# Optimization experiments

Measured on AMD Instinct MI355X. Metric: run time of the kernel, lower is better.

The kernel has to match this reference:

```python
import jax, jax.numpy as jnp
import numpy as np

B, H, W, C = 4, 64, 64, 128
C8 = C // 8  # query/key channels


def setup_inputs() -> dict:
    key = jax.random.key(0)
    ks = jax.random.split(key, 7)
    s_in = 1.0 / np.sqrt(C)
    x = jax.random.normal(ks[0], (B, H, W, C), dtype=jnp.float32)
    Wq = jax.random.normal(ks[1], (C, C8), dtype=jnp.float32) * s_in
    bq = jnp.zeros((C8,), dtype=jnp.float32)
    Wk = jax.random.normal(ks[2], (C, C8), dtype=jnp.float32) * s_in
    bk = jnp.zeros((C8,), dtype=jnp.float32)
    Wv = jax.random.normal(ks[3], (C, C), dtype=jnp.float32) * s_in
    bv = jnp.zeros((C,), dtype=jnp.float32)
    gamma = jnp.zeros((), dtype=jnp.float32)
    return {"x": x, "Wq": Wq, "bq": bq, "Wk": Wk, "bk": bk,
            "Wv": Wv, "bv": bv, "gamma": gamma}


def reference(x, Wq, bq, Wk, bk, Wv, bv, gamma):
    b, h, w, c = x.shape
    n = h * w
    xt = x.reshape(b, n, c)  # tokens
    # 1x1 convs == per-token linear projections
    q = xt @ Wq + bq          # [B, N, C/8]
    k = xt @ Wk + bk          # [B, N, C/8]
    v = xt @ Wv + bv          # [B, N, C]
    energy = jnp.einsum('bnd,bmd->bnm', q, k)   # [B, N, N]
    attention = jax.nn.softmax(energy, axis=-1)
    out = jnp.einsum('bnm,bmc->bnc', attention, v)  # [B, N, C]
    out = out.reshape(b, h, w, c)
    return out * gamma + x, attention
```

## Files before the change

kernel.cpp:

```cpp
#include <hip/hip_runtime.h>

#define B_   4
#define N_   4096
#define C_   128
#define C8_  16
#define BN_  (B_*N_)
#define SHIFT 8.0f
#define LOG2E 1.4426950408889634f

typedef _Float16 half4_t __attribute__((ext_vector_type(4)));
typedef float    f32x4   __attribute__((ext_vector_type(4)));

__global__ __launch_bounds__(256) void qkv_proj(
    const float* __restrict__ x,  const float* __restrict__ Wq,
    const float* __restrict__ bq, const float* __restrict__ Wk,
    const float* __restrict__ bk, const float* __restrict__ Wv,
    const float* __restrict__ bv, const float* __restrict__ gm,
    _Float16* __restrict__ q, _Float16* __restrict__ k,
    float* __restrict__ v, float* __restrict__ out)
{
    __shared__ float xs[16][132];
    const int tid = threadIdx.x;
    const int t0  = blockIdx.x * 16;

    {
        const int tt = tid >> 4, cs = (tid & 15) * 8;
        const float* src = x + (size_t)(t0 + tt) * C_ + cs;
        float4 a = *(const float4*)src;
        float4 b = *(const float4*)(src + 4);
        float* dst = out + (size_t)(t0 + tt) * C_ + cs;
        *(float4*)dst       = a;
        *(float4*)(dst + 4) = b;
        xs[tt][cs+0]=a.x; xs[tt][cs+1]=a.y; xs[tt][cs+2]=a.z; xs[tt][cs+3]=a.w;
        xs[tt][cs+4]=b.x; xs[tt][cs+5]=b.y; xs[tt][cs+6]=b.z; xs[tt][cs+7]=b.w;
    }
    __syncthreads();

    const int tt = tid >> 4;
    const int j  = tid & 15;

    float aq = bq[j], ak = bk[j];
    #pragma unroll 8
    for (int c = 0; c < C_; ++c) {
        float xv = xs[tt][c];
        aq = fmaf(xv, Wq[c*C8_ + j], aq);
        ak = fmaf(xv, Wk[c*C8_ + j], ak);
    }
    q[(size_t)(t0+tt)*C8_ + j] = (_Float16)(aq * LOG2E);
    k[(size_t)(t0+tt)*C8_ + j] = (_Float16)ak;

    if (gm[0] != 0.0f) {
        float av[8];
        #pragma unroll
        for (int u = 0; u < 8; ++u) av[u] = bv[j*8 + u];
        for (int c = 0; c < C_; ++c) {
            float xv = xs[tt][c];
            float4 w0 = *(const float4*)(Wv + (size_t)c*C_ + j*8);
            float4 w1 = *(const float4*)(Wv + (size_t)c*C_ + j*8 + 4);
            av[0]=fmaf(xv,w0.x,av[0]); av[1]=fmaf(xv,w0.y,av[1]);
            av[2]=fmaf(xv,w0.z,av[2]); av[3]=fmaf(xv,w0.w,av[3]);
            av[4]=fmaf(xv,w1.x,av[4]); av[5]=fmaf(xv,w1.y,av[5]);
            av[6]=fmaf(xv,w1.z,av[6]); av[7]=fmaf(xv,w1.w,av[7]);
        }
        float4* dst = (float4*)(v + (size_t)(t0+tt)*C_ + j*8);
        dst[0] = make_float4(av[0],av[1],av[2],av[3]);
        dst[1] = make_float4(av[4],av[5],av[6],av[7]);
    }
}

__global__ __launch_bounds__(256, 4) void attn_mfma(
    const _Float16* __restrict__ q, const _Float16* __restrict__ k,
    float* __restrict__ attn)
{
    __shared__ float lsum[4][16];
    const int tid  = threadIdx.x;
    const int b    = blockIdx.x >> 8;
    const int row0 = (blockIdx.x & 255) * 16;
    const int wave = tid >> 6, lane = tid & 63;
    const int rr   = lane & 15;
    const int g    = lane >> 4;

    const float ebase = -(SHIFT*LOG2E);

    const half4_t qb = *(const half4_t*)(q + (size_t)(b*N_ + row0 + rr)*C8_ + 4*g);

    const _Float16* kbase = k + (size_t)b*N_*C8_;
    const int col0 = wave * (N_/4);
    const int NT   = (N_/4)/16;
    const _Float16* kw = kbase + (size_t)(col0 + rr)*C8_ + 4*g;

    f32x4 acc4 = {0.f,0.f,0.f,0.f};
    {
        half4_t kf[8];
        #pragma unroll
        for (int i = 0; i < 8; ++i)
            kf[i] = *(const half4_t*)(kw + (size_t)i*16*C8_);
        const f32x4 cin = {ebase, ebase, ebase, ebase};
        #pragma unroll 8
        for (int s = 0; s < NT; ++s) {
            f32x4 d = __builtin_amdgcn_mfma_f32_16x16x16f16(kf[s & 7], qb, cin, 0, 0, 0);
            const int nn = (s+8 < NT) ? s+8 : NT-1;
            kf[s & 7] = *(const half4_t*)(kw + (size_t)nn*16*C8_);
            acc4[0] += __builtin_amdgcn_exp2f(d[0]);
            acc4[1] += __builtin_amdgcn_exp2f(d[1]);
            acc4[2] += __builtin_amdgcn_exp2f(d[2]);
            acc4[3] += __builtin_amdgcn_exp2f(d[3]);
        }
    }
    float acc = (acc4[0]+acc4[1]) + (acc4[2]+acc4[3]);
    acc += __shfl_xor(acc, 16);
    acc += __shfl_xor(acc, 32);
    if (lane < 16) lsum[wave][lane] = acc;
    __syncthreads();
    const float tot = (lsum[0][rr] + lsum[1][rr]) + (lsum[2][rr] + lsum[3][rr]);
    const float cstv = ebase - __builtin_amdgcn_logf(tot);

    {
        float* adst = attn + (size_t)(b*N_ + row0 + rr)*N_ + col0 + 4*g;
        half4_t kf[8];
        #pragma unroll
        for (int i = 0; i < 8; ++i)
            kf[i] = *(const half4_t*)(kw + (size_t)i*16*C8_);
        const f32x4 cin = {cstv, cstv, cstv, cstv};
        #pragma unroll 8
        for (int s = 0; s < NT; ++s) {
            f32x4 d = __builtin_amdgcn_mfma_f32_16x16x16f16(kf[s & 7], qb, cin, 0, 0, 0);
            const int nn = (s+8 < NT) ? s+8 : NT-1;
            kf[s & 7] = *(const half4_t*)(kw + (size_t)nn*16*C8_);
            f32x4 p;
            p[0] = __builtin_amdgcn_exp2f(d[0]);
            p[1] = __builtin_amdgcn_exp2f(d[1]);
            p[2] = __builtin_amdgcn_exp2f(d[2]);
            p[3] = __builtin_amdgcn_exp2f(d[3]);
            *(f32x4*)(adst + s*16) = p;
        }
    }
}

__global__ __launch_bounds__(256) void out_kernel(
    const float* __restrict__ x, const float* __restrict__ gm,
    const float* __restrict__ attn, const float* __restrict__ v,
    float* __restrict__ out)
{
    const float g = gm[0];
    if (g == 0.0f) return;
    __shared__ float sh[256];
    for (int rr = 0; rr < 8; ++rr) {
        const int row = blockIdx.x * 8 + rr;
        const int bb  = row >> 12;
        const int c   = threadIdx.x & 127;
        const int h   = threadIdx.x >> 7;
        const float* arow = attn + (size_t)row * N_;
        float acc = 0.f;
        for (int m = h*2048; m < (h+1)*2048; ++m)
            acc = fmaf(arow[m], v[(size_t)(bb*N_ + m)*C_ + c], acc);
        sh[threadIdx.x] = acc;
        __syncthreads();
        if (threadIdx.x < 128) {
            const float o = sh[threadIdx.x] + sh[threadIdx.x + 128];
            out[(size_t)row*C_ + c] = fmaf(g, o, x[(size_t)row*C_ + c]);
        }
        __syncthreads();
    }
}

extern "C" void kernel_launch(void* const* d_in, const int* in_sizes, int n_in,
                              void* d_out, int out_size, void* d_ws, size_t ws_size,
                              hipStream_t stream) {
    const float* x  = (const float*)d_in[0];
    const float* Wq = (const float*)d_in[1];
    const float* bq = (const float*)d_in[2];
    const float* Wk = (const float*)d_in[3];
    const float* bk = (const float*)d_in[4];
    const float* Wv = (const float*)d_in[5];
    const float* bv = (const float*)d_in[6];
    const float* gm = (const float*)d_in[7];

    float* out  = (float*)d_out;
    float* attn = out + (size_t)BN_ * C_;

    _Float16* q = (_Float16*)d_ws;
    _Float16* k = q + (size_t)BN_ * C8_;
    float*    v = (float*)(k + (size_t)BN_ * C8_);

    qkv_proj <<<BN_/16, 256, 0, stream>>>(x, Wq, bq, Wk, bk, Wv, bv, gm, q, k, v, out);
    attn_mfma<<<B_*(N_/16), 256, 0, stream>>>(q, k, attn);
    out_kernel<<<2048, 256, 0, stream>>>(x, gm, attn, v, out);
}
```

Measured before the change: 69.68 us.

## Split attention into separate row-sum and write kernels with more blocks

Splits the fused two-pass attention kernel into two kernels. The first computes only the softmax row sums and stores them to workspace. The second recomputes the scores and writes normalized probabilities, using twice as many blocks, and preloads all 32 key fragments per wave so the loop runs fully unrolled. This aims to raise parallelism and memory-level overlap in the write-bound phase, at the cost of an extra launch, a global row-sum round trip, and higher register pressure.

```diff
diff --git a/kernel.cpp b/kernel.cpp
--- a/kernel.cpp
+++ b/kernel.cpp
@@ -68,11 +68,11 @@
     }
 }
 
-__global__ __launch_bounds__(256, 4) void attn_mfma(
+__global__ __launch_bounds__(256, 4) void attn_rowsum(
     const _Float16* __restrict__ q, const _Float16* __restrict__ k,
-    float* __restrict__ attn)
-{
-    __shared__ float lsum[4][16];
+    float* __restrict__ lsum)
+{
+    __shared__ float ls[4][16];
     const int tid  = threadIdx.x;
     const int b    = blockIdx.x >> 8;
     const int row0 = (blockIdx.x & 255) * 16;
@@ -81,7 +81,6 @@
     const int g    = lane >> 4;
 
     const float ebase = -(SHIFT*LOG2E);
-
     const half4_t qb = *(const half4_t*)(q + (size_t)(b*N_ + row0 + rr)*C8_ + 4*g);
 
     const _Float16* kbase = k + (size_t)b*N_*C8_;
@@ -110,30 +109,48 @@
     float acc = (acc4[0]+acc4[1]) + (acc4[2]+acc4[3]);
     acc += __shfl_xor(acc, 16);
     acc += __shfl_xor(acc, 32);
-    if (lane < 16) lsum[wave][lane] = acc;
+    if (lane < 16) ls[wave][lane] = acc;
     __syncthreads();
-    const float tot = (lsum[0][rr] + lsum[1][rr]) + (lsum[2][rr] + lsum[3][rr]);
-    const float cstv = ebase - __builtin_amdgcn_logf(tot);
-
-    {
-        float* adst = attn + (size_t)(b*N_ + row0 + rr)*N_ + col0 + 4*g;
-        half4_t kf[8];
-        #pragma unroll
-        for (int i = 0; i < 8; ++i)
-            kf[i] = *(const half4_t*)(kw + (size_t)i*16*C8_);
-        const f32x4 cin = {cstv, cstv, cstv, cstv};
-        #pragma unroll 8
-        for (int s = 0; s < NT; ++s) {
-            f32x4 d = __builtin_amdgcn_mfma_f32_16x16x16f16(kf[s & 7], qb, cin, 0, 0, 0);
-            const int nn = (s+8 < NT) ? s+8 : NT-1;
-            kf[s & 7] = *(const half4_t*)(kw + (size_t)nn*16*C8_);
-            f32x4 p;
-            p[0] = __builtin_amdgcn_exp2f(d[0]);
-            p[1] = __builtin_amdgcn_exp2f(d[1]);
-            p[2] = __builtin_amdgcn_exp2f(d[2]);
-            p[3] = __builtin_amdgcn_exp2f(d[3]);
-            *(f32x4*)(adst + s*16) = p;
-        }
+    if (tid < 16)
+        lsum[b*N_ + row0 + tid] = (ls[0][tid] + ls[1][tid]) + (ls[2][tid] + ls[3][tid]);
+}
+
+__global__ __launch_bounds__(256, 4) void attn_write(
+    const _Float16* __restrict__ q, const _Float16* __restrict__ k,
+    const float* __restrict__ lsum, float* __restrict__ attn)
+{
+    const int tid  = threadIdx.x;
+    const int bid  = blockIdx.x;
+    const int b    = bid >> 9;
+    const int rem  = bid & 511;
+    const int row0 = (rem >> 1) * 16;
+    const int ch   = rem & 1;
+    const int wave = tid >> 6, lane = tid & 63;
+    const int rr   = lane & 15;
+    const int g    = lane >> 4;
+    const int col0 = ch*2048 + wave*512;
+
+    const half4_t qb = *(const half4_t*)(q + (size_t)(b*N_ + row0 + rr)*C8_ + 4*g);
+    const float tot  = lsum[b*N_ + row0 + rr];
+    const float cstv = -(SHIFT*LOG2E) - __builtin_amdgcn_logf(tot);
+    const f32x4 cin  = {cstv, cstv, cstv, cstv};
+
+    const _Float16* kw = k + ((size_t)b*N_ + col0 + rr)*C8_ + 4*g;
+    half4_t kf[32];
+    #pragma unroll
+    for (int i = 0; i < 32; ++i)
+        kf[i] = *(const half4_t*)(kw + (size_t)i*16*C8_);
+
+    float* adst = attn + (size_t)(b*N_ + row0 + rr)*N_ + col0 + 4*g;
+    #pragma unroll
+    for (int s = 0; s < 32; ++s) {
+        f32x4 d = __builtin_amdgcn_mfma_f32_16x16x16f16(kf[s], qb, cin, 0, 0, 0);
+        f32x4 p;
+        p[0] = __builtin_amdgcn_exp2f(d[0]);
+        p[1] = __builtin_amdgcn_exp2f(d[1]);
+        p[2] = __builtin_amdgcn_exp2f(d[2]);
+        p[3] = __builtin_amdgcn_exp2f(d[3]);
+        *(f32x4*)(adst + s*16) = p;
     }
 }
 
@@ -182,8 +199,10 @@
     _Float16* q = (_Float16*)d_ws;
     _Float16* k = q + (size_t)BN_ * C8_;
     float*    v = (float*)(k + (size_t)BN_ * C8_);
-
-    qkv_proj <<<BN_/16, 256, 0, stream>>>(x, Wq, bq, Wk, bk, Wv, bv, gm, q, k, v, out);
-    attn_mfma<<<B_*(N_/16), 256, 0, stream>>>(q, k, attn);
-    out_kernel<<<2048, 256, 0, stream>>>(x, gm, attn, v, out);
-}
+    float*    lsum = v + (size_t)BN_ * C_;
+
+    qkv_proj   <<<BN_/16, 256, 0, stream>>>(x, Wq, bq, Wk, bk, Wv, bv, gm, q, k, v, out);
+    attn_rowsum<<<B_*(N_/16), 256, 0, stream>>>(q, k, lsum);
+    attn_write <<<2*B_*(N_/16), 256, 0, stream>>>(q, k, lsum, attn);
+    out_kernel <<<2048, 256, 0, stream>>>(x, gm, attn, v, out);
+}
```

Result: slower. 71.76 us (+3.0%).
